# Performance work log

Hardware: AMD Instinct MI355X
Metric: run time of the kernel (lower is better)

The kernel has to match this reference:

```python
import jax, jax.numpy as jnp
import numpy as np

N = 100000
E = 1200000
D = 64
EPS = 0.1
GAMMA = 0.1


def gcn_conv(x, row, col, norm, phiW, n):
    # GCNConv(bias=False): xW then normalized sum aggregation (self-loops already in row/col)
    xw = x @ phiW.T                                   # [N, D]
    msg = xw[row] * norm[:, None]                     # [E+N, D] gather + scale
    return jax.ops.segment_sum(msg, col, num_segments=n)


def antisym_conv(x, row, col, norm, W, phiW, b):
    n, d = x.shape
    aW = W - W.T - GAMMA * jnp.eye(d, dtype=x.dtype)  # antisymmetric part minus gamma*I
    h = jnp.tanh(x @ aW.T + gcn_conv(x, row, col, norm, phiW, n) + b)
    return x + EPS * h                                # num_iters = 1


def _prep_edges(edge_index, n, dtype):
    # add self loops (fill weight 1.0) and compute symmetric GCN normalization
    loop = jnp.arange(n, dtype=edge_index.dtype)
    row = jnp.concatenate([edge_index[0], loop])
    col = jnp.concatenate([edge_index[1], loop])
    deg = jax.ops.segment_sum(jnp.ones(row.shape, dtype), col, num_segments=n)
    dinv = jnp.where(deg > 0, jax.lax.rsqrt(deg), 0.0)
    norm = dinv[row] * dinv[col]
    return row, col, norm


def setup_inputs() -> dict:
    key = jax.random.key(0)
    ks = jax.random.split(key, 10)
    s = 1.0 / np.sqrt(D)
    return {
        "x": jax.random.normal(ks[0], (N, D), jnp.float32),
        "W1": jax.random.uniform(ks[1], (D, D), jnp.float32, -s, s),
        "phiW1": jax.random.uniform(ks[2], (D, D), jnp.float32, -s, s),
        "b1": jax.random.uniform(ks[3], (D,), jnp.float32, -s, s),
        "W2": jax.random.uniform(ks[4], (D, D), jnp.float32, -s, s),
        "phiW2": jax.random.uniform(ks[5], (D, D), jnp.float32, -s, s),
        "b2": jax.random.uniform(ks[6], (D,), jnp.float32, -s, s),
        "outW": jax.random.uniform(ks[7], (1, D), jnp.float32, -s, s),
        "outb": jax.random.uniform(ks[8], (1,), jnp.float32, -s, s),
        "edge_index": jax.random.randint(ks[9], (2, E), 0, N, jnp.int64 if jax.config.jax_enable_x64 else jnp.int32),
    }


def reference(x, W1, phiW1, b1, W2, phiW2, b2, outW, outb, edge_index):
    row, col, norm = _prep_edges(edge_index, x.shape[0], x.dtype)
    x = jnp.maximum(antisym_conv(x, row, col, norm, W1, phiW1, b1), 0.0)
    x = jnp.maximum(antisym_conv(x, row, col, norm, W2, phiW2, b2), 0.0)
    return (x @ outW.T + outb)[:, 0]  # squeeze(-1)
```

## Files before the change

kernel.cpp:

```cpp
#include <hip/hip_runtime.h>
#include <math.h>

#define DD 64
static constexpr float GAMMA_C = 0.1f;
static constexpr float EPS_C = 0.1f;

__global__ __launch_bounds__(256) void k_prep(const float* __restrict__ W1,
                                              const float* __restrict__ phiW1,
                                              const float* __restrict__ W2,
                                              const float* __restrict__ phiW2,
                                              float* __restrict__ aWT1,
                                              float* __restrict__ phiWT1,
                                              float* __restrict__ aWT2,
                                              float* __restrict__ phiWT2) {
  int idx = blockIdx.x * 256 + threadIdx.x;
  if (idx >= 4096) return;
  int k = idx >> 6, j = idx & 63;
  float g = (j == k) ? GAMMA_C : 0.f;
  aWT1[idx] = W1[j * 64 + k] - W1[k * 64 + j] - g;
  aWT2[idx] = W2[j * 64 + k] - W2[k * 64 + j] - g;
  phiWT1[idx] = phiW1[j * 64 + k];
  phiWT2[idx] = phiW2[j * 64 + k];
}

__global__ __launch_bounds__(256) void k_hist(const int* __restrict__ col,
                                              int* __restrict__ hist, int e) {
  int i = blockIdx.x * blockDim.x + threadIdx.x;
  int stride = gridDim.x * blockDim.x;
  for (; i < e; i += stride) atomicAdd(&hist[col[i]], 1);
}

__global__ __launch_bounds__(256) void k_scan1(const int* __restrict__ hist,
                                               int* __restrict__ rs,
                                               int* __restrict__ bsum, int n) {
  __shared__ int wtot[4];
  int b = blockIdx.x, t = threadIdx.x;
  int base = b * 2048 + t * 8;
  int v[8];
  int s = 0;
#pragma unroll
  for (int u = 0; u < 8; ++u) {
    int idx = base + u;
    v[u] = (idx < n) ? hist[idx] : 0;
    s += v[u];
  }
  int lane = t & 63, wid = t >> 6;
  int ws = s;
#pragma unroll
  for (int d = 1; d < 64; d <<= 1) {
    int o = __shfl_up(ws, d);
    if (lane >= d) ws += o;
  }
  if (lane == 63) wtot[wid] = ws;
  __syncthreads();
  int off = 0;
  for (int w = 0; w < wid; ++w) off += wtot[w];
  int run = ws - s + off;
#pragma unroll
  for (int u = 0; u < 8; ++u) {
    int idx = base + u;
    if (idx < n) rs[idx] = run;
    run += v[u];
  }
  if (t == 255) bsum[b] = run;
}

__global__ void k_scan2(const int* __restrict__ bsum, int* __restrict__ boff,
                        int nb, int* __restrict__ rs, int n, int e) {
  int t = threadIdx.x;
  int v = (t < nb) ? bsum[t] : 0;
  int s = v;
#pragma unroll
  for (int d = 1; d < 64; d <<= 1) {
    int o = __shfl_up(s, d);
    if (t >= d) s += o;
  }
  if (t < nb) boff[t] = s - v;
  if (t == 0) rs[n] = e;
}

__global__ __launch_bounds__(256) void k_scan3_dinv(int* __restrict__ rs,
                                                    const int* __restrict__ boff,
                                                    const int* __restrict__ hist,
                                                    float* __restrict__ dinv, int n) {
  int i = blockIdx.x * blockDim.x + threadIdx.x;
  if (i < n) {
    rs[i] += boff[i >> 11];
    dinv[i] = rsqrtf((float)(hist[i] + 1));
  }
}

__global__ __launch_bounds__(256) void k_fill(const int* __restrict__ row,
                                              const int* __restrict__ col,
                                              const int* __restrict__ rs,
                                              int* __restrict__ fillc,
                                              const float* __restrict__ dinv,
                                              int2* __restrict__ csr, int e) {
  int i = blockIdx.x * blockDim.x + threadIdx.x;
  int stride = gridDim.x * blockDim.x;
  for (; i < e; i += stride) {
    int c = col[i];
    int r = row[i];
    int p = atomicAdd(&fillc[c], 1);
    csr[rs[c] + p] = make_int2(r, __float_as_int(dinv[r]));
  }
}

__global__ __launch_bounds__(256) void k_xw(const float* __restrict__ x,
                                            const float* __restrict__ phiWT,
                                            float* __restrict__ xw, int n) {
  int lane = threadIdx.x & 63;
  int gw = __builtin_amdgcn_readfirstlane(
      (int)((blockIdx.x * blockDim.x + threadIdx.x) >> 6));
  int nw = (gridDim.x * blockDim.x) >> 6;
  float w[64];
#pragma unroll
  for (int k = 0; k < 64; ++k) w[k] = phiWT[k * 64 + lane];
  for (int i = gw; i < n; i += nw) {
    const float* xr = x + (size_t)i * DD;
    float a0 = 0.f, a1 = 0.f, a2 = 0.f, a3 = 0.f;
#pragma unroll
    for (int k = 0; k < 64; k += 4) {
      a0 = fmaf(xr[k + 0], w[k + 0], a0);
      a1 = fmaf(xr[k + 1], w[k + 1], a1);
      a2 = fmaf(xr[k + 2], w[k + 2], a2);
      a3 = fmaf(xr[k + 3], w[k + 3], a3);
    }
    xw[(size_t)i * DD + lane] = (a0 + a1) + (a2 + a3);
  }
}

template <bool FINAL>
__global__ __launch_bounds__(256) void k_agg(const float* __restrict__ xin,
                                             const float* __restrict__ xw,
                                             const float* __restrict__ aWT,
                                             const float* __restrict__ b,
                                             const int2* __restrict__ csr,
                                             const int* __restrict__ rs,
                                             const float* __restrict__ dinv,
                                             const float* __restrict__ outW,
                                             const float* __restrict__ outb,
                                             float* __restrict__ xo,
                                             float* __restrict__ out, int n) {
  int lane = threadIdx.x & 63;
  int gw = __builtin_amdgcn_readfirstlane(
      (int)((blockIdx.x * blockDim.x + threadIdx.x) >> 6));
  int nw = (gridDim.x * blockDim.x) >> 6;
  float w[64];
#pragma unroll
  for (int k = 0; k < 64; ++k) w[k] = aWT[k * 64 + lane];
  float bj = b[lane];
  float ow = FINAL ? outW[lane] : 0.f;
  for (int i = gw; i < n; i += nw) {
    int s = rs[i];
    int t = rs[i + 1];
    float dvc = dinv[i];
    size_t o = (size_t)i * DD + lane;
    float a0 = dvc * xw[o];
    float a1 = 0.f, a2 = 0.f, a3 = 0.f;
    int k = s;
    for (; k + 3 < t; k += 4) {
      int2 e0 = csr[k], e1 = csr[k + 1], e2 = csr[k + 2], e3 = csr[k + 3];
      a0 = fmaf(xw[(size_t)e0.x * DD + lane], __int_as_float(e0.y), a0);
      a1 = fmaf(xw[(size_t)e1.x * DD + lane], __int_as_float(e1.y), a1);
      a2 = fmaf(xw[(size_t)e2.x * DD + lane], __int_as_float(e2.y), a2);
      a3 = fmaf(xw[(size_t)e3.x * DD + lane], __int_as_float(e3.y), a3);
    }
    for (; k < t; ++k) {
      int2 e0 = csr[k];
      a0 = fmaf(xw[(size_t)e0.x * DD + lane], __int_as_float(e0.y), a0);
    }
    float aggr = dvc * ((a0 + a1) + (a2 + a3));
    const float* xr = xin + (size_t)i * DD;
    float l0 = 0.f, l1 = 0.f, l2 = 0.f, l3 = 0.f;
#pragma unroll
    for (int kk = 0; kk < 64; kk += 4) {
      l0 = fmaf(xr[kk + 0], w[kk + 0], l0);
      l1 = fmaf(xr[kk + 1], w[kk + 1], l1);
      l2 = fmaf(xr[kk + 2], w[kk + 2], l2);
      l3 = fmaf(xr[kk + 3], w[kk + 3], l3);
    }
    float tot = ((l0 + l1) + (l2 + l3)) + bj + aggr;
    float val = fmaxf(fmaf(EPS_C, tanhf(tot), xin[o]), 0.f);
    if (FINAL) {
      float p = val * ow;
#pragma unroll
      for (int sg = 32; sg > 0; sg >>= 1) p += __shfl_xor(p, sg);
      if (lane == 0) out[i] = p + outb[0];
    } else {
      xo[o] = val;
    }
  }
}

extern "C" void kernel_launch(void* const* d_in, const int* in_sizes, int n_in,
                              void* d_out, int out_size, void* d_ws, size_t ws_size,
                              hipStream_t stream) {
  const float* x     = (const float*)d_in[0];
  const float* W1    = (const float*)d_in[1];
  const float* phiW1 = (const float*)d_in[2];
  const float* b1    = (const float*)d_in[3];
  const float* W2    = (const float*)d_in[4];
  const float* phiW2 = (const float*)d_in[5];
  const float* b2    = (const float*)d_in[6];
  const float* outW  = (const float*)d_in[7];
  const float* outb  = (const float*)d_in[8];
  const int*   ei    = (const int*)d_in[9];

  int n = in_sizes[0] / DD;
  int e = in_sizes[9] / 2;
  const int* row = ei;
  const int* col = ei + e;
  float* out = (float*)d_out;

  char* w = (char*)d_ws;
  auto carve = [&](size_t bytes) {
    char* p = w;
    w += (bytes + 255) & ~(size_t)255;
    return p;
  };
  float* aWT1   = (float*)carve(4096 * 4);
  float* phiWT1 = (float*)carve(4096 * 4);
  float* aWT2   = (float*)carve(4096 * 4);
  float* phiWT2 = (float*)carve(4096 * 4);
  int*   hist   = (int*)carve((size_t)n * 4);
  int*   fillc  = (int*)carve((size_t)n * 4);
  int*   rs     = (int*)carve(((size_t)n + 1) * 4);
  int*   bsum   = (int*)carve(64 * 4);
  int*   boff   = (int*)carve(64 * 4);
  float* dinv   = (float*)carve((size_t)n * 4);
  int2*  csr    = (int2*)carve((size_t)e * 8);
  float* xw     = (float*)carve((size_t)n * DD * 4);
  float* x1     = (float*)carve((size_t)n * DD * 4);

  int nb_n   = (n + 255) / 256;
  int nb_e   = 2048;
  int nb_sc1 = (n + 2047) / 2048;
  int nb_xw  = 1024;
  int nb_ag  = 2048;

  size_t zbytes = (size_t)((char*)fillc - (char*)hist) + (size_t)n * 4;
  hipMemsetAsync(hist, 0, zbytes, stream);

  k_prep<<<16, 256, 0, stream>>>(W1, phiW1, W2, phiW2, aWT1, phiWT1, aWT2, phiWT2);
  k_hist<<<nb_e, 256, 0, stream>>>(col, hist, e);
  k_scan1<<<nb_sc1, 256, 0, stream>>>(hist, rs, bsum, n);
  k_scan2<<<1, 64, 0, stream>>>(bsum, boff, nb_sc1, rs, n, e);
  k_scan3_dinv<<<nb_n, 256, 0, stream>>>(rs, boff, hist, dinv, n);
  k_fill<<<nb_e, 256, 0, stream>>>(row, col, rs, fillc, dinv, csr, e);

  k_xw<<<nb_xw, 256, 0, stream>>>(x, phiWT1, xw, n);
  k_agg<false><<<nb_ag, 256, 0, stream>>>(x, xw, aWT1, b1, csr, rs, dinv,
                                          nullptr, nullptr, x1, nullptr, n);

  k_xw<<<nb_xw, 256, 0, stream>>>(x1, phiWT2, xw, n);
  k_agg<true><<<nb_ag, 256, 0, stream>>>(x1, xw, aWT2, b2, csr, rs, dinv,
                                         outW, outb, nullptr, out, n);
}
```

Before: 475.0 us.

## Fold source dinv into xw, shrink CSR to int, process node pairs per wave

Scales each xw row by its dinv when the row is produced, so CSR entries no longer carry a per-edge weight. This halves CSR storage and the bytes read in the gather loop. The aggregation kernel now handles two adjacent destination nodes per wave over one merged edge range, unrolled by 8 with a select mask, to raise memory-level parallelism. Launch bounds now request 4 blocks per SIMD, which caps register use with the 64-float weight array. The cost is the extra masked FMA per edge and possible register spills.

Result: slower. 496.9 us (+4.6%).

```diff
diff --git a/kernel.cpp b/kernel.cpp
--- a/kernel.cpp
+++ b/kernel.cpp
@@ -94,21 +94,21 @@
                                               const int* __restrict__ col,
                                               const int* __restrict__ rs,
                                               int* __restrict__ fillc,
-                                              const float* __restrict__ dinv,
-                                              int2* __restrict__ csr, int e) {
+                                              int* __restrict__ csr, int e) {
   int i = blockIdx.x * blockDim.x + threadIdx.x;
   int stride = gridDim.x * blockDim.x;
   for (; i < e; i += stride) {
     int c = col[i];
     int r = row[i];
     int p = atomicAdd(&fillc[c], 1);
-    csr[rs[c] + p] = make_int2(r, __float_as_int(dinv[r]));
-  }
-}
-
-__global__ __launch_bounds__(256) void k_xw(const float* __restrict__ x,
-                                            const float* __restrict__ phiWT,
-                                            float* __restrict__ xw, int n) {
+    csr[rs[c] + p] = r;
+  }
+}
+
+__global__ __launch_bounds__(256, 4) void k_xw(const float* __restrict__ x,
+                                               const float* __restrict__ phiWT,
+                                               const float* __restrict__ dinv,
+                                               float* __restrict__ xw, int n) {
   int lane = threadIdx.x & 63;
   int gw = __builtin_amdgcn_readfirstlane(
       (int)((blockIdx.x * blockDim.x + threadIdx.x) >> 6));
@@ -118,6 +118,7 @@
   for (int k = 0; k < 64; ++k) w[k] = phiWT[k * 64 + lane];
   for (int i = gw; i < n; i += nw) {
     const float* xr = x + (size_t)i * DD;
+    float dv = dinv[i];
     float a0 = 0.f, a1 = 0.f, a2 = 0.f, a3 = 0.f;
 #pragma unroll
     for (int k = 0; k < 64; k += 4) {
@@ -126,22 +127,22 @@
       a2 = fmaf(xr[k + 2], w[k + 2], a2);
       a3 = fmaf(xr[k + 3], w[k + 3], a3);
     }
-    xw[(size_t)i * DD + lane] = (a0 + a1) + (a2 + a3);
+    xw[(size_t)i * DD + lane] = dv * ((a0 + a1) + (a2 + a3));
   }
 }
 
 template <bool FINAL>
-__global__ __launch_bounds__(256) void k_agg(const float* __restrict__ xin,
-                                             const float* __restrict__ xw,
-                                             const float* __restrict__ aWT,
-                                             const float* __restrict__ b,
-                                             const int2* __restrict__ csr,
-                                             const int* __restrict__ rs,
-                                             const float* __restrict__ dinv,
-                                             const float* __restrict__ outW,
-                                             const float* __restrict__ outb,
-                                             float* __restrict__ xo,
-                                             float* __restrict__ out, int n) {
+__global__ __launch_bounds__(256, 4) void k_agg(const float* __restrict__ xin,
+                                                const float* __restrict__ xw,
+                                                const float* __restrict__ aWT,
+                                                const float* __restrict__ b,
+                                                const int* __restrict__ csr,
+                                                const int* __restrict__ rs,
+                                                const float* __restrict__ dinv,
+                                                const float* __restrict__ outW,
+                                                const float* __restrict__ outb,
+                                                float* __restrict__ xo,
+                                                float* __restrict__ out, int n) {
   int lane = threadIdx.x & 63;
   int gw = __builtin_amdgcn_readfirstlane(
       (int)((blockIdx.x * blockDim.x + threadIdx.x) >> 6));
@@ -151,44 +152,79 @@
   for (int k = 0; k < 64; ++k) w[k] = aWT[k * 64 + lane];
   float bj = b[lane];
   float ow = FINAL ? outW[lane] : 0.f;
-  for (int i = gw; i < n; i += nw) {
+  for (int i = 2 * gw; i < n; i += 2 * nw) {
+    bool hasB = (i + 1) < n;
     int s = rs[i];
-    int t = rs[i + 1];
-    float dvc = dinv[i];
-    size_t o = (size_t)i * DD + lane;
-    float a0 = dvc * xw[o];
-    float a1 = 0.f, a2 = 0.f, a3 = 0.f;
+    int mid = rs[i + 1];
+    int t = hasB ? rs[i + 2] : mid;
+    size_t oA = (size_t)i * DD + lane;
+    size_t oB = oA + DD;
+    float accA[4] = {xw[oA], 0.f, 0.f, 0.f};
+    float accB[4] = {hasB ? xw[oB] : 0.f, 0.f, 0.f, 0.f};
     int k = s;
-    for (; k + 3 < t; k += 4) {
-      int2 e0 = csr[k], e1 = csr[k + 1], e2 = csr[k + 2], e3 = csr[k + 3];
-      a0 = fmaf(xw[(size_t)e0.x * DD + lane], __int_as_float(e0.y), a0);
-      a1 = fmaf(xw[(size_t)e1.x * DD + lane], __int_as_float(e1.y), a1);
-      a2 = fmaf(xw[(size_t)e2.x * DD + lane], __int_as_float(e2.y), a2);
-      a3 = fmaf(xw[(size_t)e3.x * DD + lane], __int_as_float(e3.y), a3);
+    for (; k + 7 < t; k += 8) {
+      int r[8];
+#pragma unroll
+      for (int u = 0; u < 8; ++u) r[u] = csr[k + u];
+      float v[8];
+#pragma unroll
+      for (int u = 0; u < 8; ++u) v[u] = xw[(size_t)r[u] * DD + lane];
+#pragma unroll
+      for (int u = 0; u < 8; ++u) {
+        float sA = (k + u < mid) ? 1.f : 0.f;
+        accA[u & 3] = fmaf(v[u], sA, accA[u & 3]);
+        accB[u & 3] = fmaf(v[u], 1.f - sA, accB[u & 3]);
+      }
     }
     for (; k < t; ++k) {
-      int2 e0 = csr[k];
-      a0 = fmaf(xw[(size_t)e0.x * DD + lane], __int_as_float(e0.y), a0);
-    }
-    float aggr = dvc * ((a0 + a1) + (a2 + a3));
-    const float* xr = xin + (size_t)i * DD;
-    float l0 = 0.f, l1 = 0.f, l2 = 0.f, l3 = 0.f;
-#pragma unroll
-    for (int kk = 0; kk < 64; kk += 4) {
-      l0 = fmaf(xr[kk + 0], w[kk + 0], l0);
-      l1 = fmaf(xr[kk + 1], w[kk + 1], l1);
-      l2 = fmaf(xr[kk + 2], w[kk + 2], l2);
-      l3 = fmaf(xr[kk + 3], w[kk + 3], l3);
-    }
-    float tot = ((l0 + l1) + (l2 + l3)) + bj + aggr;
-    float val = fmaxf(fmaf(EPS_C, tanhf(tot), xin[o]), 0.f);
-    if (FINAL) {
-      float p = val * ow;
-#pragma unroll
-      for (int sg = 32; sg > 0; sg >>= 1) p += __shfl_xor(p, sg);
-      if (lane == 0) out[i] = p + outb[0];
-    } else {
-      xo[o] = val;
+      float v = xw[(size_t)csr[k] * DD + lane];
+      float sA = (k < mid) ? 1.f : 0.f;
+      accA[0] = fmaf(v, sA, accA[0]);
+      accB[0] = fmaf(v, 1.f - sA, accB[0]);
+    }
+    {
+      float aggr = dinv[i] * ((accA[0] + accA[1]) + (accA[2] + accA[3]));
+      const float* xr = xin + (size_t)i * DD;
+      float l0 = 0.f, l1 = 0.f, l2 = 0.f, l3 = 0.f;
+#pragma unroll
+      for (int kk = 0; kk < 64; kk += 4) {
+        l0 = fmaf(xr[kk + 0], w[kk + 0], l0);
+        l1 = fmaf(xr[kk + 1], w[kk + 1], l1);
+        l2 = fmaf(xr[kk + 2], w[kk + 2], l2);
+        l3 = fmaf(xr[kk + 3], w[kk + 3], l3);
+      }
+      float tot = ((l0 + l1) + (l2 + l3)) + bj + aggr;
+      float val = fmaxf(fmaf(EPS_C, tanhf(tot), xin[oA]), 0.f);
+      if (FINAL) {
+        float p = val * ow;
+#pragma unroll
+        for (int sg = 32; sg > 0; sg >>= 1) p += __shfl_xor(p, sg);
+        if (lane == 0) out[i] = p + outb[0];
+      } else {
+        xo[oA] = val;
+      }
+    }
+    if (hasB) {
+      float aggr = dinv[i + 1] * ((accB[0] + accB[1]) + (accB[2] + accB[3]));
+      const float* xr = xin + (size_t)(i + 1) * DD;
+      float l0 = 0.f, l1 = 0.f, l2 = 0.f, l3 = 0.f;
+#pragma unroll
+      for (int kk = 0; kk < 64; kk += 4) {
+        l0 = fmaf(xr[kk + 0], w[kk + 0], l0);
+        l1 = fmaf(xr[kk + 1], w[kk + 1], l1);
+        l2 = fmaf(xr[kk + 2], w[kk + 2], l2);
+        l3 = fmaf(xr[kk + 3], w[kk + 3], l3);
+      }
+      float tot = ((l0 + l1) + (l2 + l3)) + bj + aggr;
+      float val = fmaxf(fmaf(EPS_C, tanhf(tot), xin[oB]), 0.f);
+      if (FINAL) {
+        float p = val * ow;
+#pragma unroll
+        for (int sg = 32; sg > 0; sg >>= 1) p += __shfl_xor(p, sg);
+        if (lane == 0) out[i + 1] = p + outb[0];
+      } else {
+        xo[oB] = val;
+      }
     }
   }
 }
@@ -229,7 +265,7 @@
   int*   bsum   = (int*)carve(64 * 4);
   int*   boff   = (int*)carve(64 * 4);
   float* dinv   = (float*)carve((size_t)n * 4);
-  int2*  csr    = (int2*)carve((size_t)e * 8);
+  int*   csr    = (int*)carve((size_t)e * 4);
   float* xw     = (float*)carve((size_t)n * DD * 4);
   float* x1     = (float*)carve((size_t)n * DD * 4);
 
@@ -247,13 +283,13 @@
   k_scan1<<<nb_sc1, 256, 0, stream>>>(hist, rs, bsum, n);
   k_scan2<<<1, 64, 0, stream>>>(bsum, boff, nb_sc1, rs, n, e);
   k_scan3_dinv<<<nb_n, 256, 0, stream>>>(rs, boff, hist, dinv, n);
-  k_fill<<<nb_e, 256, 0, stream>>>(row, col, rs, fillc, dinv, csr, e);
-
-  k_xw<<<nb_xw, 256, 0, stream>>>(x, phiWT1, xw, n);
+  k_fill<<<nb_e, 256, 0, stream>>>(row, col, rs, fillc, csr, e);
+
+  k_xw<<<nb_xw, 256, 0, stream>>>(x, phiWT1, dinv, xw, n);
   k_agg<false><<<nb_ag, 256, 0, stream>>>(x, xw, aWT1, b1, csr, rs, dinv,
                                           nullptr, nullptr, x1, nullptr, n);
 
-  k_xw<<<nb_xw, 256, 0, stream>>>(x1, phiWT2, xw, n);
+  k_xw<<<nb_xw, 256, 0, stream>>>(x1, phiWT2, dinv, xw, n);
   k_agg<true><<<nb_ag, 256, 0, stream>>>(x1, xw, aWT2, b2, csr, rs, dinv,
                                          outW, outb, nullptr, out, n);
 }
```
